# Kernel optimization log

Hardware: AMD Instinct MI355X
Metric: run time of the kernel (lower is better)

## Reference

```python
import jax, jax.numpy as jnp
import numpy as np

DIM = 512
HEADS = 8
DIM_HEAD = 64
INNER = HEADS * DIM_HEAD  # 512
B, N = 32, 512
LN_EPS = 1e-5


def setup_inputs() -> dict:
    key = jax.random.key(0)
    ks = jax.random.split(key, 8)
    inp = {
        "q": jax.random.normal(ks[0], (B, N, DIM), jnp.float32),
        "k": jax.random.normal(ks[1], (B, N, DIM), jnp.float32),
        "v": jax.random.normal(ks[2], (B, N, DIM), jnp.float32),
        "ln_w": jnp.ones((DIM,), jnp.float32),
        "ln_b": jnp.zeros((DIM,), jnp.float32),
        "W_in": jax.random.normal(ks[3], (DIM, INNER), jnp.float32) / np.sqrt(DIM),
        "W_out": jax.random.normal(ks[4], (INNER, DIM), jnp.float32) / np.sqrt(INNER),
        "b_out": jnp.zeros((DIM,), jnp.float32),
        "cov_w_raw": jnp.float32(0.6),
        "var_w_raw": jnp.float32(0.2),
    }
    return inp


def _project(x, ln_w, ln_b, W_in):
    # LayerNorm(dim) -> Linear(dim, inner, bias=False) -> 'b n (h d) -> h b n d'
    mu = jnp.mean(x, axis=-1, keepdims=True)
    var = jnp.var(x, axis=-1, keepdims=True)  # biased, as in nn.LayerNorm
    xn = (x - mu) / jnp.sqrt(var + LN_EPS) * ln_w + ln_b
    f = xn @ W_in  # [B, N, inner]
    Bq, Nq, _ = f.shape
    f = f.reshape(Bq, Nq, HEADS, DIM_HEAD)
    return jnp.transpose(f, (2, 0, 1, 3))  # [h, B, N, d]


def reference(q, k, v, ln_w, ln_b, W_in, W_out, b_out, cov_w_raw, var_w_raw):
    f_q = _project(q, ln_w, ln_b, W_in)  # [h, B, N, d]
    f_k = _project(k, ln_w, ln_b, W_in)
    f_v = _project(v, ln_w, ln_b, W_in)

    d = f_q.shape[-1]

    # cosine similarity: (q . k) / (||q|| ||k||)
    dots = jnp.einsum('hbnd,hbmd->hbnm', f_q, f_k)
    qn = jnp.linalg.norm(f_q, axis=-1)  # [h, B, N]
    kn = jnp.linalg.norm(f_k, axis=-1)  # [h, B, M]
    cosine_sim = dots / (qn[..., :, None] * kn[..., None, :])

    # basic covariance component: centered dot / d
    qc = f_q - jnp.mean(f_q, axis=-1, keepdims=True)
    kc = f_k - jnp.mean(f_k, axis=-1, keepdims=True)
    cov_component = jnp.einsum('hbnd,hbmd->hbnm', qc, kc) / d

    # variance component: outer product of per-token variances (unbiased) / d
    q_var = jnp.var(f_q, axis=-1, ddof=1)  # [h, B, N]
    k_var = jnp.var(f_k, axis=-1, ddof=1)  # [h, B, M]
    var_component = (q_var[..., :, None] * k_var[..., None, :]) / d

    cov_w = jax.nn.sigmoid(cov_w_raw)
    var_w = jax.nn.sigmoid(var_w_raw)
    cos_w = 1.0 - cov_w - var_w

    scores = cos_w * cosine_sim + cov_w * cov_component + var_w * var_component
    out = jnp.einsum('hbnm,hbmd->hbnd', scores, f_v)  # no softmax in cosine variant

    # 'h b n d -> b n (h d)'
    out = jnp.transpose(out, (1, 2, 0, 3)).reshape(out.shape[1], out.shape[2], INNER)
    return out @ W_out + b_out
```

## Files before the change

kernel.cpp:

```cpp
#include <hip/hip_runtime.h>
#include <stdint.h>

using u16 = unsigned short;
using u32 = unsigned int;
using bf16x8 = __bf16 __attribute__((ext_vector_type(8)));
using f32x4  = float __attribute__((ext_vector_type(4)));

__device__ __forceinline__ float bflo(u32 u){ return __uint_as_float(u << 16); }
__device__ __forceinline__ float bfhi(u32 u){ return __uint_as_float(u & 0xffff0000u); }
__device__ __forceinline__ u16 f2bf(float f){
  u32 u = __float_as_uint(f);
  u += 0x7fffu + ((u >> 16) & 1u);
  return (u16)(u >> 16);
}
__device__ __forceinline__ u32 pk2(float a, float b){
  return (u32)f2bf(a) | ((u32)f2bf(b) << 16);
}
__device__ __forceinline__ void gload16(const void* g, void* l){
  __builtin_amdgcn_global_load_lds(
      (const __attribute__((address_space(1))) void*)(uintptr_t)(g),
      (__attribute__((address_space(3))) void*)(uintptr_t)(l), 16, 0, 0);
}

__global__ __launch_bounds__(256) void prep_k(const float* __restrict__ Win,
                                              const float* __restrict__ Wout,
                                              const float* __restrict__ lnw,
                                              const float* __restrict__ lnb,
                                              u16* __restrict__ WpT,
                                              u16* __restrict__ WoutT,
                                              float* __restrict__ g1,
                                              float* __restrict__ g2){
  __shared__ float tile[32][33];
  __shared__ float red[2][8][32];
  int bid = blockIdx.x;
  if (bid < 512){
    int bz = bid >> 8, bi = bid & 255;
    int bx = bi & 15, by = bi >> 4;
    const float* src = bz ? Wout : Win;
    u16* dst = bz ? WoutT : WpT;
    int tx = threadIdx.x & 31, ty = threadIdx.x >> 5;
    int c0 = bx * 32, r0 = by * 32;
#pragma unroll
    for (int i = 0; i < 4; ++i)
      tile[ty + i*8][tx] = src[(size_t)(r0 + ty + i*8)*512 + c0 + tx];
    __syncthreads();
    float sc = bz ? 1.f : lnw[r0 + tx];
#pragma unroll
    for (int i = 0; i < 4; ++i)
      dst[(size_t)(c0 + ty + i*8)*512 + r0 + tx] = f2bf(tile[tx][ty + i*8] * sc);
  } else {
    int bi = bid - 512;
    int col = bi*32 + (threadIdx.x & 31);
    int s = threadIdx.x >> 5;
    float p1 = 0.f, p2 = 0.f;
    for (int kk = 0; kk < 64; ++kk){
      int k = s*64 + kk;
      float wv = Win[(size_t)k*512 + col];
      p1 += lnw[k]*wv; p2 += lnb[k]*wv;
    }
    red[0][s][threadIdx.x & 31] = p1;
    red[1][s][threadIdx.x & 31] = p2;
    __syncthreads();
    if (threadIdx.x < 32){
      float a1 = 0.f, a2 = 0.f;
#pragma unroll
      for (int s2 = 0; s2 < 8; ++s2){ a1 += red[0][s2][threadIdx.x]; a2 += red[1][s2][threadIdx.x]; }
      g1[bi*32 + threadIdx.x] = a1;
      g2[bi*32 + threadIdx.x] = a2;
    }
  }
}

template<int ORIENT, int FSTAT>
__device__ __forceinline__ void proj_body(
    const float* __restrict__ X, const u16* __restrict__ Wp,
    const float* __restrict__ g1, const float* __restrict__ g2,
    u16* __restrict__ C, float* __restrict__ fstat, int ldC, int bid,
    char* sW, char* sX, float* sF){
  float* sMu = sF;        float* sRs = sF + 128;
  float* sG1 = sF + 256;  float* sG2 = sF + 384;
  const int t = threadIdx.x, w = t >> 6, l = t & 63;
  const int wr = w >> 1, wc = w & 1;
  const int lr = l & 15, lg = l >> 4;
  int bx, by;
  if (ORIENT == 0){ bx = bid & 127; by = bid >> 7; }
  else { int j = bid >> 3; bx = j & 3; by = (bid & 7) + 8*(j >> 2); }
  const int row0 = bx * 128, col0 = by * 128;
  const int xbase = (ORIENT == 0) ? row0 : col0;
  const int wbase = (ORIENT == 0) ? col0 : row0;

  const int sc = t >> 3, k8 = t & 7;
  const int sso = (k8*16) ^ ((sc & 7) << 4);
  const char* Wpp = (const char*)Wp + ((size_t)(wbase + sc) << 10) + sso;
  const float* Xp = X + ((size_t)(xbase + sc) << 9) + k8*8;

  if (t < 128){ sG1[t] = g1[wbase + t]; sG2[t] = g2[wbase + t]; }

  float xr[4][8];
  float psum[4] = {}, pss[4] = {};
  f32x4 acc[4][4] = {};

  auto XLOAD = [&](int kt){
#pragma unroll
    for (int ii = 0; ii < 4; ++ii){
      const float* p = Xp + ii*(32*512) + kt*64;
      float4 a = *(const float4*)p, c4 = *(const float4*)(p + 4);
      xr[ii][0]=a.x;  xr[ii][1]=a.y;  xr[ii][2]=a.z;  xr[ii][3]=a.w;
      xr[ii][4]=c4.x; xr[ii][5]=c4.y; xr[ii][6]=c4.z; xr[ii][7]=c4.w;
    }
  };
  auto XWRITE = [&](){
#pragma unroll
    for (int ii = 0; ii < 4; ++ii){
#pragma unroll
      for (int e = 0; e < 8; ++e){ psum[ii] += xr[ii][e]; pss[ii] += xr[ii][e]*xr[ii][e]; }
      uint4 pk;
      pk.x = pk2(xr[ii][0], xr[ii][1]); pk.y = pk2(xr[ii][2], xr[ii][3]);
      pk.z = pk2(xr[ii][4], xr[ii][5]); pk.w = pk2(xr[ii][6], xr[ii][7]);
      *(uint4*)(sX + (sc + ii*32)*128 + sso) = pk;
    }
  };
  auto WSTAGE = [&](int kt){
#pragma unroll
    for (int ii = 0; ii < 4; ++ii)
      gload16(Wpp + (size_t)ii*32768 + kt*128, sW + ii*4096 + w*1024);
  };

  XLOAD(0);
  for (int kt = 0; kt < 8; ++kt){
    WSTAGE(kt);
    XWRITE();
    asm volatile("s_waitcnt vmcnt(0) lgkmcnt(0)" ::: "memory");
    __builtin_amdgcn_s_barrier();
    __builtin_amdgcn_sched_barrier(0);
    if (kt < 7) XLOAD(kt + 1);
    __builtin_amdgcn_sched_barrier(0);
    const char* aB = (ORIENT == 0) ? sX : sW;
    const char* bB = (ORIENT == 0) ? sW : sX;
#pragma unroll
    for (int kk = 0; kk < 2; ++kk){
      bf16x8 af[4], bfg[4];
#pragma unroll
      for (int m = 0; m < 4; ++m){
        int r = wr*64 + m*16 + lr;
        af[m] = *(const bf16x8*)(aB + r*128 + ((kk*64 + lg*16) ^ ((r & 7) << 4)));
      }
#pragma unroll
      for (int n = 0; n < 4; ++n){
        int r = wc*64 + n*16 + lr;
        bfg[n] = *(const bf16x8*)(bB + r*128 + ((kk*64 + lg*16) ^ ((r & 7) << 4)));
      }
#pragma unroll
      for (int m = 0; m < 4; ++m)
#pragma unroll
        for (int n = 0; n < 4; ++n)
          acc[m][n] = __builtin_amdgcn_mfma_f32_16x16x32_bf16(af[m], bfg[n], acc[m][n], 0, 0, 0);
    }
    asm volatile("s_waitcnt lgkmcnt(0)" ::: "memory");
    __builtin_amdgcn_s_barrier();
    __builtin_amdgcn_sched_barrier(0);
  }

#pragma unroll
  for (int ii = 0; ii < 4; ++ii){
    float s = psum[ii], s2 = pss[ii];
#pragma unroll
    for (int off = 1; off < 8; off <<= 1){ s += __shfl_xor(s, off); s2 += __shfl_xor(s2, off); }
    if (k8 == 0){
      float mu = s * (1.f/512.f);
      sMu[sc + ii*32] = mu;
      sRs[sc + ii*32] = rsqrtf(s2 * (1.f/512.f) - mu*mu + 1e-5f);
    }
  }
  __syncthreads();

  float cs[4] = {}, cs2[4] = {};
#pragma unroll
  for (int m = 0; m < 4; ++m){
#pragma unroll
    for (int q = 0; q < 4; ++q){
      int ri = wr*64 + m*16 + lg*4 + q;
      float rsv = 0.f, muv = 0.f, g1r = 0.f, g2r = 0.f;
      if (ORIENT == 0){ rsv = sRs[ri]; muv = sMu[ri]; }
      else { g1r = sG1[ri]; g2r = sG2[ri]; }
      float fv[4];
#pragma unroll
      for (int n = 0; n < 4; ++n){
        int ci = wc*64 + n*16 + lr;
        float a = acc[m][n][q];
        if (ORIENT == 0) fv[n] = rsv*(a - muv*sG1[ci]) + sG2[ci];
        else             fv[n] = sRs[ci]*(a - sMu[ci]*g1r) + g2r;
        C[(size_t)(row0 + ri)*ldC + (col0 + ci)] = f2bf(fv[n]);
        if (FSTAT == 2){ cs[n] += fv[n]; cs2[n] += fv[n]*fv[n]; }
      }
      if (FSTAT == 1){
        float s  = (fv[0]+fv[1]) + (fv[2]+fv[3]);
        float s2 = (fv[0]*fv[0]+fv[1]*fv[1]) + (fv[2]*fv[2]+fv[3]*fv[3]);
#pragma unroll
        for (int off = 1; off < 16; off <<= 1){ s += __shfl_xor(s, off); s2 += __shfl_xor(s2, off); }
        if (lr == 0){
          int head = (col0 >> 6) + wc;
          *(float2*)(fstat + ((size_t)(row0 + ri)*8 + head)*2) = make_float2(s, s2);
        }
      }
    }
  }
  if (FSTAT == 2){
    int head = (row0 >> 6) + wr;
#pragma unroll
    for (int n = 0; n < 4; ++n){
      float s = cs[n], s2 = cs2[n];
      s += __shfl_xor(s, 16); s2 += __shfl_xor(s2, 16);
      s += __shfl_xor(s, 32); s2 += __shfl_xor(s2, 32);
      if (lg == 0){
        int tok = col0 + wc*64 + n*16 + lr;
        *(float2*)(fstat + ((size_t)tok*8 + head)*2) = make_float2(s, s2);
      }
    }
  }
}

__global__ __launch_bounds__(256, 3) void proj_k(
    const float* __restrict__ q, const float* __restrict__ k, const float* __restrict__ v,
    const u16* __restrict__ Wp, const float* __restrict__ g1, const float* __restrict__ g2,
    u16* __restrict__ fq, u16* __restrict__ kT, u16* __restrict__ vT,
    float* __restrict__ qstat, float* __restrict__ kstat){
  __shared__ __align__(16) char sW[16384];
  __shared__ __align__(16) char sX[16384];
  __shared__ float sF[512];
  int bid = blockIdx.x;
  if (bid < 512)
    proj_body<0,1>(q, Wp, g1, g2, fq, qstat, 512, bid, sW, sX, sF);
  else if (bid < 1024)
    proj_body<1,2>(k, Wp, g1, g2, kT, kstat, 16384, bid - 512, sW, sX, sF);
  else
    proj_body<1,0>(v, Wp, g1, g2, vT, nullptr, 16384, bid - 1024, sW, sX, sF);
}

__global__ __launch_bounds__(256) void outgemm_k(
    const u16* __restrict__ A, const u16* __restrict__ B,
    float* __restrict__ Cf, const float* __restrict__ bias){
  __shared__ __align__(16) char sA[16384];
  __shared__ __align__(16) char sB[16384];
  const int t = threadIdx.x, w = t >> 6, l = t & 63;
  const int wr = w >> 1, wc = w & 1;
  const int lr = l & 15, lg = l >> 4;
  const int row0 = blockIdx.x * 128, col0 = blockIdx.y * 128;
  f32x4 acc[4][4] = {};

  const int sc = t >> 3, k8 = t & 7;
  const int sso = (k8*16) ^ ((sc & 7) << 4);
  const char* Ap = (const char*)A + ((size_t)(row0 + sc) << 10) + sso;
  const char* Bp = (const char*)B + ((size_t)(col0 + sc) << 10) + sso;

  for (int kt = 0; kt < 8; ++kt){
    __syncthreads();
#pragma unroll
    for (int ii = 0; ii < 4; ++ii){
      gload16(Ap + (size_t)ii*32768 + kt*128, sA + ii*4096 + w*1024);
      gload16(Bp + (size_t)ii*32768 + kt*128, sB + ii*4096 + w*1024);
    }
    __syncthreads();
#pragma unroll
    for (int kk = 0; kk < 2; ++kk){
      bf16x8 af[4], bfg[4];
#pragma unroll
      for (int m = 0; m < 4; ++m){
        int r = wr*64 + m*16 + lr;
        af[m] = *(const bf16x8*)(sA + r*128 + ((kk*64 + lg*16) ^ ((r & 7) << 4)));
      }
#pragma unroll
      for (int n = 0; n < 4; ++n){
        int r = wc*64 + n*16 + lr;
        bfg[n] = *(const bf16x8*)(sB + r*128 + ((kk*64 + lg*16) ^ ((r & 7) << 4)));
      }
#pragma unroll
      for (int m = 0; m < 4; ++m)
#pragma unroll
        for (int n = 0; n < 4; ++n)
          acc[m][n] = __builtin_amdgcn_mfma_f32_16x16x32_bf16(af[m], bfg[n], acc[m][n], 0, 0, 0);
    }
  }
#pragma unroll
  for (int m = 0; m < 4; ++m){
#pragma unroll
    for (int q = 0; q < 4; ++q){
      int r = row0 + wr*64 + m*16 + lg*4 + q;
#pragma unroll
      for (int n = 0; n < 4; ++n){
        int cc = col0 + wc*64 + n*16 + lr;
        Cf[(size_t)r*512 + cc] = acc[m][n][q] + bias[cc];
      }
    }
  }
}

__global__ __launch_bounds__(512) void attn_k(
    const u16* __restrict__ fq, const u16* __restrict__ kT, const u16* __restrict__ vT,
    const float* __restrict__ qstat, const float* __restrict__ kstat,
    u16* __restrict__ ao,
    const float* __restrict__ cwr, const float* __restrict__ vwr){
  __shared__ __align__(16) char smem[131072 + 1664*4];
  float* sStat = (float*)(smem + 131072);
  float* sS1 = sStat + 1536;
  float* sS2 = sStat + 1600;

  const int t = threadIdx.x, w = t >> 6, l = t & 63;
  const int lr = l & 15, lg = l >> 4;
  const int h = blockIdx.x & 7, b = blockIdx.x >> 3;

  float cwv = 1.f/(1.f + __expf(-*cwr));
  float vwv = 1.f/(1.f + __expf(-*vwr));
  float cosw = 1.f - cwv - vwv;

  const char* kTb = (const char*)kT + (size_t)h*64*32768 + (size_t)b*1024;
  const char* vTb = (const char*)vT + (size_t)h*64*32768 + (size_t)b*1024;
#pragma unroll
  for (int ii = 0; ii < 8; ++ii){
    int c = ii*512 + t, d = c >> 6, u = c & 63;
    int so = d*32768 + ((u ^ (d & 7)) << 4);
    gload16(kTb + so, smem + ii*8192 + w*1024);
    gload16(vTb + so, smem + 65536 + ii*8192 + w*1024);
  }
  {
    float2 ksr = *(const float2*)(kstat + ((size_t)(b*512 + t)*8 + h)*2);
    float mk = ksr.x * (1.f/64.f);
    sStat[t]        = rsqrtf(ksr.y);
    sStat[512 + t]  = mk;
    sStat[1024 + t] = (ksr.y - 64.f*mk*mk) * (1.f/63.f);
  }
  __syncthreads();

  const int jt = (w >> 1), itp = (w & 1);
  f32x4 m2acc[2] = {}, m1acc[2] = {};
  {
    const int j = jt*16 + lr;
#pragma unroll
    for (int ks = 0; ks < 16; ++ks){
      int u = ks*4 + lg;
      bf16x8 af = *(const bf16x8*)(smem + 65536 + j*1024 + ((u ^ (j & 7)) << 4));
#pragma unroll
      for (int tt = 0; tt < 2; ++tt){
        int i = (itp*2 + tt)*16 + lr;
        bf16x8 bf = *(const bf16x8*)(smem + i*1024 + ((u ^ (i & 7)) << 4));
        m2acc[tt] = __builtin_amdgcn_mfma_f32_16x16x32_bf16(af, bf, m2acc[tt], 0, 0, 0);
      }
    }
  }
  {
    int j = t >> 3, g = t & 7;
    float p1 = 0.f, p2 = 0.f;
#pragma unroll
    for (int uu = 0; uu < 8; ++uu){
      int ut = g*8 + uu;
      uint4 uv = *(const uint4*)(smem + 65536 + j*1024 + ((ut ^ (j & 7)) << 4));
      int m0 = ut*8;
      float4 mk0 = *(const float4*)(sStat + 512 + m0);
      float4 mk1 = *(const float4*)(sStat + 512 + m0 + 4);
      float4 kv0 = *(const float4*)(sStat + 1024 + m0);
      float4 kv1 = *(const float4*)(sStat + 1024 + m0 + 4);
      float v0=bflo(uv.x),v1=bfhi(uv.x),v2=bflo(uv.y),v3=bfhi(uv.y);
      float v4=bflo(uv.z),v5=bfhi(uv.z),v6=bflo(uv.w),v7=bfhi(uv.w);
      p1 += v0*mk0.x + v1*mk0.y + v2*mk0.z + v3*mk0.w
          + v4*mk1.x + v5*mk1.y + v6*mk1.z + v7*mk1.w;
      p2 += v0*kv0.x + v1*kv0.y + v2*kv0.z + v3*kv0.w
          + v4*kv1.x + v5*kv1.y + v6*kv1.z + v7*kv1.w;
    }
#pragma unroll
    for (int off = 1; off < 8; off <<= 1){ p1 += __shfl_xor(p1, off); p2 += __shfl_xor(p2, off); }
    if (g == 0){ sS1[j] = p1; sS2[j] = p2; }
  }
  __syncthreads();

#pragma unroll
  for (int ii = 0; ii < 32; ++ii){
    int wd = ii*512 + t;
    int d = wd >> 8, o = wd & 255, ud = o >> 2, p = o & 3;
    int m0 = ((ud ^ (d & 7)) << 3) + p*2;
    u32 uv = *(u32*)(smem + wd*4);
    *(u32*)(smem + wd*4) = pk2(bflo(uv)*sStat[m0], bfhi(uv)*sStat[m0+1]);
  }
  __syncthreads();

  {
    const int j = jt*16 + lr;
#pragma unroll
    for (int ks = 0; ks < 16; ++ks){
      int u = ks*4 + lg;
      bf16x8 af = *(const bf16x8*)(smem + 65536 + j*1024 + ((u ^ (j & 7)) << 4));
#pragma unroll
      for (int tt = 0; tt < 2; ++tt){
        int i = (itp*2 + tt)*16 + lr;
        bf16x8 bf = *(const bf16x8*)(smem + i*1024 + ((u ^ (i & 7)) << 4));
        m1acc[tt] = __builtin_amdgcn_mfma_f32_16x16x32_bf16(af, bf, m1acc[tt], 0, 0, 0);
      }
    }
  }
  __syncthreads();

#pragma unroll
  for (int tt = 0; tt < 2; ++tt){
#pragma unroll
    for (int q = 0; q < 4; ++q){
      int j = jt*16 + lg*4 + q;
      int i = (itp*2 + tt)*16 + lr;
      int bo = j*128 + (((i >> 3) ^ (j & 7)) << 4) + (i & 7)*2;
      *(u16*)(smem + bo)        = f2bf(m1acc[tt][q]);
      *(u16*)(smem + 8192 + bo) = f2bf(m2acc[tt][q]);
    }
  }
  const char* fqb = (const char*)fq + (size_t)b*524288 + h*128;
#pragma unroll
  for (int ii = 0; ii < 8; ++ii){
    int c = ii*512 + t, n = c >> 3, u = c & 7;
    gload16(fqb + n*1024 + ((u ^ (n & 7)) << 4), smem + 65536 + ii*8192 + w*1024);
  }
  __syncthreads();

  float s1v[4], s2v[4];
#pragma unroll
  for (int nt = 0; nt < 4; ++nt){ s1v[nt] = sS1[nt*16 + lr]; s2v[nt] = sS2[nt*16 + lr]; }
  const float Bc = cwv * (1.f/64.f);

#pragma unroll
  for (int mt = 0; mt < 4; ++mt){
    f32x4 a1[4] = {}, a2[4] = {};
    const int n = w*64 + mt*16 + lr;
#pragma unroll
    for (int kk = 0; kk < 2; ++kk){
      int u = kk*4 + lg;
      bf16x8 af = *(const bf16x8*)(smem + 65536 + n*128 + ((u ^ (n & 7)) << 4));
#pragma unroll
      for (int nt = 0; nt < 4; ++nt){
        int j = nt*16 + lr;
        bf16x8 b1 = *(const bf16x8*)(smem + j*128 + ((u ^ (j & 7)) << 4));
        bf16x8 b2 = *(const bf16x8*)(smem + 8192 + j*128 + ((u ^ (j & 7)) << 4));
        a1[nt] = __builtin_amdgcn_mfma_f32_16x16x32_bf16(af, b1, a1[nt], 0, 0, 0);
        a2[nt] = __builtin_amdgcn_mfma_f32_16x16x32_bf16(af, b2, a2[nt], 0, 0, 0);
      }
    }
#pragma unroll
    for (int q = 0; q < 4; ++q){
      int nr = w*64 + mt*16 + lg*4 + q;
      float2 qs = *(const float2*)(qstat + ((size_t)(b*512 + nr)*8 + h)*2);
      float mq = qs.x * (1.f/64.f);
      float An = cosw * rsqrtf(qs.y);
      float Cn = -cwv * mq;
      float En = vwv * (1.f/64.f) * ((qs.y - 64.f*mq*mq) * (1.f/63.f));
      char* op = (char*)ao + ((size_t)(b*512 + nr)*512 + h*64)*2;
#pragma unroll
      for (int nt = 0; nt < 4; ++nt){
        float ov = An*a1[nt][q] + Bc*a2[nt][q] + Cn*s1v[nt] + En*s2v[nt];
        *(u16*)(op + (nt*16 + lr)*2) = f2bf(ov);
      }
    }
  }
}

extern "C" void kernel_launch(void* const* d_in, const int* in_sizes, int n_in,
                              void* d_out, int out_size, void* d_ws, size_t ws_size,
                              hipStream_t stream){
  const float* q    = (const float*)d_in[0];
  const float* k    = (const float*)d_in[1];
  const float* v    = (const float*)d_in[2];
  const float* lnw  = (const float*)d_in[3];
  const float* lnb  = (const float*)d_in[4];
  const float* Win  = (const float*)d_in[5];
  const float* Wout = (const float*)d_in[6];
  const float* bout = (const float*)d_in[7];
  const float* cwr  = (const float*)d_in[8];
  const float* vwr  = (const float*)d_in[9];

  char* ws = (char*)d_ws;
  const size_t FB = (size_t)16384 * 512 * 2;
  u16* fq  = (u16*)(ws);
  u16* kT  = (u16*)(ws + FB);
  u16* vT  = (u16*)(ws + 2*FB);
  u16* ao  = (u16*)(ws + 3*FB);
  u16* WpT   = (u16*)(ws + 4*FB);
  u16* WoutT = (u16*)(ws + 4*FB + 524288);
  float* g1  = (float*)(ws + 4*FB + 1048576);
  float* g2  = (float*)(ws + 4*FB + 1048576 + 2048);
  float* qstat = (float*)d_out;
  float* kstat = qstat + 262144;

  prep_k<<<528, 256, 0, stream>>>(Win, Wout, lnw, lnb, WpT, WoutT, g1, g2);

  proj_k<<<1536, 256, 0, stream>>>(q, k, v, WpT, g1, g2, fq, kT, vT, qstat, kstat);

  attn_k<<<256, 512, 0, stream>>>(fq, kT, vT, qstat, kstat, ao, cwr, vwr);

  outgemm_k<<<dim3(128,4), 256, 0, stream>>>(ao, WoutT, (float*)d_out, bout);
}
```

Baseline: 98.89 us.

## Multi-buffer output GEMM loads with a four-stage async LDS pipeline

Rewrites the output projection GEMM to use a four-slot LDS ring with K-tiles of 32, issuing global-to-LDS loads three stages ahead and using explicit vmcnt waits plus one barrier per step in place of two syncthreads per tile. It also changes the LDS swizzle layout, flattens the grid to 1D, and swaps the software bf16 pack for the hardware v_cvt_pk_bf16_f32 instruction. The goal is to hide global load latency behind MFMA work. The trade-offs are 64KB of LDS per block, which lowers occupancy, and the fact that correctness now depends on hand-counted vmcnt values.

```diff
diff --git a/kernel.cpp b/kernel.cpp
--- a/kernel.cpp
+++ b/kernel.cpp
@@ -14,7 +14,9 @@
   return (u16)(u >> 16);
 }
 __device__ __forceinline__ u32 pk2(float a, float b){
-  return (u32)f2bf(a) | ((u32)f2bf(b) << 16);
+  u32 r;
+  asm("v_cvt_pk_bf16_f32 %0, %1, %2" : "=v"(r) : "v"(a), "v"(b));
+  return r;
 }
 __device__ __forceinline__ void gload16(const void* g, void* l){
   __builtin_amdgcn_global_load_lds(
@@ -240,56 +242,65 @@
 __global__ __launch_bounds__(256) void outgemm_k(
     const u16* __restrict__ A, const u16* __restrict__ B,
     float* __restrict__ Cf, const float* __restrict__ bias){
-  __shared__ __align__(16) char sA[16384];
-  __shared__ __align__(16) char sB[16384];
+  __shared__ __align__(16) char sM[65536];
   const int t = threadIdx.x, w = t >> 6, l = t & 63;
   const int wr = w >> 1, wc = w & 1;
   const int lr = l & 15, lg = l >> 4;
-  const int row0 = blockIdx.x * 128, col0 = blockIdx.y * 128;
+  const int bx = blockIdx.x & 127, by = blockIdx.x >> 7;
+  const int row0 = bx*128, col0 = by*128;
+
+  const int spr = t >> 3, se = (t & 7) ^ (spr & 7);
+  const int srow = spr*2 + (se >> 2), sk16 = se & 3;
+  const char* Ap0 = (const char*)A + ((size_t)(row0 + srow) << 10) + sk16*16;
+  const char* Bp0 = (const char*)B + ((size_t)(col0 + srow) << 10) + sk16*16;
+  const int ldst = w*1024 + l*16;
+
+  const int qf = ((((lr & 1) << 2) | lg) ^ ((lr >> 1) & 7)) * 16;
+  const int afb = wr*4096 + (lr >> 1)*128 + qf;
+  const int bfb = wc*4096 + (lr >> 1)*128 + qf;
+
   f32x4 acc[4][4] = {};
 
-  const int sc = t >> 3, k8 = t & 7;
-  const int sso = (k8*16) ^ ((sc & 7) << 4);
-  const char* Ap = (const char*)A + ((size_t)(row0 + sc) << 10) + sso;
-  const char* Bp = (const char*)B + ((size_t)(col0 + sc) << 10) + sso;
-
-  for (int kt = 0; kt < 8; ++kt){
-    __syncthreads();
-#pragma unroll
-    for (int ii = 0; ii < 4; ++ii){
-      gload16(Ap + (size_t)ii*32768 + kt*128, sA + ii*4096 + w*1024);
-      gload16(Bp + (size_t)ii*32768 + kt*128, sB + ii*4096 + w*1024);
-    }
-    __syncthreads();
-#pragma unroll
-    for (int kk = 0; kk < 2; ++kk){
-      bf16x8 af[4], bfg[4];
-#pragma unroll
-      for (int m = 0; m < 4; ++m){
-        int r = wr*64 + m*16 + lr;
-        af[m] = *(const bf16x8*)(sA + r*128 + ((kk*64 + lg*16) ^ ((r & 7) << 4)));
-      }
-#pragma unroll
-      for (int n = 0; n < 4; ++n){
-        int r = wc*64 + n*16 + lr;
-        bfg[n] = *(const bf16x8*)(sB + r*128 + ((kk*64 + lg*16) ^ ((r & 7) << 4)));
-      }
-#pragma unroll
-      for (int m = 0; m < 4; ++m)
-#pragma unroll
-        for (int n = 0; n < 4; ++n)
-          acc[m][n] = __builtin_amdgcn_mfma_f32_16x16x32_bf16(af[m], bfg[n], acc[m][n], 0, 0, 0);
-    }
-  }
+  auto STAGE = [&](int kt, int buf){
+    char* d = sM + buf*16384;
+    gload16(Ap0 + kt*64,         d + ldst);
+    gload16(Ap0 + 65536 + kt*64, d + 4096 + ldst);
+    gload16(Bp0 + kt*64,         d + 8192 + ldst);
+    gload16(Bp0 + 65536 + kt*64, d + 12288 + ldst);
+  };
+
+  STAGE(0, 0); STAGE(1, 1); STAGE(2, 2);
+#pragma unroll
+  for (int kt = 0; kt < 16; ++kt){
+    if (kt < 14)       asm volatile("s_waitcnt vmcnt(8)" ::: "memory");
+    else if (kt == 14) asm volatile("s_waitcnt vmcnt(4)" ::: "memory");
+    else               asm volatile("s_waitcnt vmcnt(0)" ::: "memory");
+    __builtin_amdgcn_s_barrier();
+    __builtin_amdgcn_sched_barrier(0);
+    if (kt < 13) STAGE(kt + 3, (kt + 3) & 3);
+    const char* aR = sM + (kt & 3)*16384;
+    const char* bR = aR + 8192;
+    bf16x8 af[4], bfg[4];
+#pragma unroll
+    for (int m = 0; m < 4; ++m) af[m]  = *(const bf16x8*)(aR + afb + m*1024);
+#pragma unroll
+    for (int n = 0; n < 4; ++n) bfg[n] = *(const bf16x8*)(bR + bfb + n*1024);
+#pragma unroll
+    for (int m = 0; m < 4; ++m)
+#pragma unroll
+      for (int n = 0; n < 4; ++n)
+        acc[m][n] = __builtin_amdgcn_mfma_f32_16x16x32_bf16(af[m], bfg[n], acc[m][n], 0, 0, 0);
+  }
+
 #pragma unroll
   for (int m = 0; m < 4; ++m){
 #pragma unroll
-    for (int q = 0; q < 4; ++q){
-      int r = row0 + wr*64 + m*16 + lg*4 + q;
+    for (int qq = 0; qq < 4; ++qq){
+      int r = row0 + wr*64 + m*16 + lg*4 + qq;
 #pragma unroll
       for (int n = 0; n < 4; ++n){
         int cc = col0 + wc*64 + n*16 + lr;
-        Cf[(size_t)r*512 + cc] = acc[m][n][q] + bias[cc];
+        Cf[(size_t)r*512 + cc] = acc[m][n][qq] + bias[cc];
       }
     }
   }
@@ -490,5 +501,5 @@
 
   attn_k<<<256, 512, 0, stream>>>(fq, kT, vT, qstat, kstat, ao, cwr, vwr);
 
-  outgemm_k<<<dim3(128,4), 256, 0, stream>>>(ao, WoutT, (float*)d_out, bout);
-}
+  outgemm_k<<<512, 256, 0, stream>>>(ao, WoutT, (float*)d_out, bout);
+}
```

Result: faster. 95.57 us (median of 3 runs) (-3.4%).
